# Optimization experiments

Measured on AMD Instinct MI355X. Metric: run time of the kernel, lower is better.

## Reference

```python
import jax, jax.numpy as jnp
import numpy as np

B, N, M, NF = 8, 512, 100, 42
DIMS = [NF, 256, 128, 64, 1]


def setup_inputs() -> dict:
    key = jax.random.key(0)
    ks = jax.random.split(key, 3 + len(DIMS) - 1)
    inp = {
        "image": jax.random.normal(ks[0], (B, N, NF), jnp.float32),
        "dfeat": jax.random.normal(ks[1], (B, N, M, NF, 3), jnp.float32) * 0.1,
        "neighbor": jax.random.randint(ks[2], (B, N, M), 0, N + 1),  # 0 = no neighbor, else 1-based atom idx
    }
    for l in range(len(DIMS) - 1):
        inp[f"W{l}"] = jax.random.normal(ks[3 + l], (DIMS[l], DIMS[l + 1]), jnp.float32) / np.sqrt(DIMS[l])
        inp[f"b{l}"] = jnp.zeros((DIMS[l + 1],), jnp.float32)
    return inp


def _atom_energy(x, Ws, bs):
    # per-atom MLP: sigmoid hidden layers, linear scalar output
    h = x
    for W, b in zip(Ws[:-1], bs[:-1]):
        h = jax.nn.sigmoid(h @ W + b)
    return (h @ Ws[-1] + bs[-1])[0]


def reference(image, dfeat, neighbor, W0, b0, W1, b1, W2, b2, W3, b3):
    Ws = (W0, W1, W2, W3)
    bs = (b0, b1, b2, b3)
    nb, na, nf = image.shape

    e_fn = lambda x: _atom_energy(x, Ws, bs)
    flat = image.reshape(-1, nf)
    Ei = jax.vmap(e_fn)(flat).reshape(nb, na)                      # [B, N]
    dE = jax.vmap(jax.grad(e_fn))(flat).reshape(nb, na, nf)        # dEi/dFeat, [B, N, F]
    Etot = jnp.sum(Ei, axis=1, keepdims=True)                      # [B, 1]

    # Force[b,i,:] = sum_m dE[b, neighbor[b,i,m]-1, :] @ dfeat[b,i,m,:,:], masking pad (0) entries
    mask = (neighbor > 0).astype(dE.dtype)                         # [B, N, M]
    idx = jnp.maximum(neighbor - 1, 0)                             # [B, N, M]
    dE_g = jax.vmap(lambda d, i: d[i])(dE, idx)                    # [B, N, M, F]
    Force = jnp.einsum('bnmf,bnmfd->bnd', dE_g * mask[..., None], dfeat)  # [B, N, 3]
    return Etot, Ei, Force
```

## Files before the change

### kernel.cpp

```cpp
#include <hip/hip_runtime.h>

#define NFEAT 42
#define H1 256
#define H2 128
#define H3 64
#define NB 8
#define NA 512
#define NM 100
#define TA 8

__device__ __forceinline__ float sigmoidf(float z) {
    return 1.0f / (1.0f + __expf(-z));
}

__global__ __launch_bounds__(256) void transpose_weights(
    const float* __restrict__ W0, const float* __restrict__ W1, const float* __restrict__ W2,
    float* __restrict__ W0T, float* __restrict__ W1T, float* __restrict__ W2T)
{
    int i = blockIdx.x * 256 + threadIdx.x;
    if (i < NFEAT * H1) {
        int f = i / H1, k = i - f * H1;
        W0T[k * NFEAT + f] = W0[i];
    }
    if (i < H1 * H2) {
        int k = i / H2, j = i - k * H2;
        W1T[j * H1 + k] = W1[i];
    }
    if (i < H2 * H3) {
        int j = i / H3, k = i - j * H3;
        W2T[k * H2 + j] = W2[i];
    }
}

__global__ __launch_bounds__(256) void mlp_fwd_bwd(
    const float* __restrict__ image,
    const float* __restrict__ W0, const float* __restrict__ b0,
    const float* __restrict__ W1, const float* __restrict__ b1,
    const float* __restrict__ W2, const float* __restrict__ b2,
    const float* __restrict__ W3, const float* __restrict__ b3,
    const float* __restrict__ W0T, const float* __restrict__ W1T, const float* __restrict__ W2T,
    float* __restrict__ Ei,
    float* __restrict__ dE)
{
    const int t = threadIdx.x;
    const int atom0 = blockIdx.x * TA;

    __shared__ float sx[TA][NFEAT];
    __shared__ __align__(16) float sh1[TA][H1];
    __shared__ __align__(16) float sh2[TA][H2];
    __shared__ __align__(16) float sh3[TA][H3];
    __shared__ __align__(16) float sd3[TA][H3];
    __shared__ __align__(16) float sd2[TA][H2];
    __shared__ __align__(16) float sd1[TA][H1];

    for (int i = t; i < TA * NFEAT; i += 256) {
        int a = i / NFEAT, f = i - a * NFEAT;
        sx[a][f] = image[(atom0 + a) * NFEAT + f];
    }
    __syncthreads();

    {
        float acc[TA];
        #pragma unroll
        for (int a = 0; a < TA; ++a) acc[a] = 0.f;
        for (int k = 0; k < NFEAT; ++k) {
            float w = W0[k * H1 + t];
            #pragma unroll
            for (int a = 0; a < TA; ++a) acc[a] += sx[a][k] * w;
        }
        float bb = b0[t];
        #pragma unroll
        for (int a = 0; a < TA; ++a) sh1[a][t] = sigmoidf(acc[a] + bb);
    }
    __syncthreads();

    {
        const int j = t & 127, g = t >> 7, a0 = g * 4;
        float acc[4] = {0.f, 0.f, 0.f, 0.f};
        for (int kk = 0; kk < H1 / 4; ++kk) {
            float w0_ = W1[(4 * kk + 0) * H2 + j];
            float w1_ = W1[(4 * kk + 1) * H2 + j];
            float w2_ = W1[(4 * kk + 2) * H2 + j];
            float w3_ = W1[(4 * kk + 3) * H2 + j];
            #pragma unroll
            for (int a = 0; a < 4; ++a) {
                float4 h = ((const float4*)sh1[a0 + a])[kk];
                acc[a] += h.x * w0_ + h.y * w1_ + h.z * w2_ + h.w * w3_;
            }
        }
        float bb = b1[j];
        #pragma unroll
        for (int a = 0; a < 4; ++a) sh2[a0 + a][j] = sigmoidf(acc[a] + bb);
    }
    __syncthreads();

    {
        const int j = t & 63, g = t >> 6, a0 = g * 2;
        float acc[2] = {0.f, 0.f};
        for (int kk = 0; kk < H2 / 4; ++kk) {
            float w0_ = W2[(4 * kk + 0) * H3 + j];
            float w1_ = W2[(4 * kk + 1) * H3 + j];
            float w2_ = W2[(4 * kk + 2) * H3 + j];
            float w3_ = W2[(4 * kk + 3) * H3 + j];
            #pragma unroll
            for (int a = 0; a < 2; ++a) {
                float4 h = ((const float4*)sh2[a0 + a])[kk];
                acc[a] += h.x * w0_ + h.y * w1_ + h.z * w2_ + h.w * w3_;
            }
        }
        float bb = b2[j];
        #pragma unroll
        for (int a = 0; a < 2; ++a) sh3[a0 + a][j] = sigmoidf(acc[a] + bb);
    }
    __syncthreads();

    {
        const int lane = t & 63, wv = t >> 6, a0 = wv * 2;
        float w = W3[lane];
        float bb = b3[0];
        #pragma unroll
        for (int a = a0; a < a0 + 2; ++a) {
            float h = sh3[a][lane];
            sd3[a][lane] = w * h * (1.f - h);
            float v = w * h;
            #pragma unroll
            for (int off = 32; off > 0; off >>= 1) v += __shfl_down(v, off, 64);
            if (lane == 0) Ei[atom0 + a] = v + bb;
        }
    }
    __syncthreads();

    {
        const int j = t & 127, g = t >> 7, a0 = g * 4;
        float acc[4] = {0.f, 0.f, 0.f, 0.f};
        for (int kk = 0; kk < H3 / 4; ++kk) {
            float w0_ = W2T[(4 * kk + 0) * H2 + j];
            float w1_ = W2T[(4 * kk + 1) * H2 + j];
            float w2_ = W2T[(4 * kk + 2) * H2 + j];
            float w3_ = W2T[(4 * kk + 3) * H2 + j];
            #pragma unroll
            for (int a = 0; a < 4; ++a) {
                float4 d = ((const float4*)sd3[a0 + a])[kk];
                acc[a] += d.x * w0_ + d.y * w1_ + d.z * w2_ + d.w * w3_;
            }
        }
        #pragma unroll
        for (int a = 0; a < 4; ++a) {
            float h = sh2[a0 + a][j];
            sd2[a0 + a][j] = acc[a] * h * (1.f - h);
        }
    }
    __syncthreads();

    {
        float acc[TA];
        #pragma unroll
        for (int a = 0; a < TA; ++a) acc[a] = 0.f;
        for (int jj = 0; jj < H2 / 4; ++jj) {
            float w0_ = W1T[(4 * jj + 0) * H1 + t];
            float w1_ = W1T[(4 * jj + 1) * H1 + t];
            float w2_ = W1T[(4 * jj + 2) * H1 + t];
            float w3_ = W1T[(4 * jj + 3) * H1 + t];
            #pragma unroll
            for (int a = 0; a < TA; ++a) {
                float4 d = ((const float4*)sd2[a])[jj];
                acc[a] += d.x * w0_ + d.y * w1_ + d.z * w2_ + d.w * w3_;
            }
        }
        #pragma unroll
        for (int a = 0; a < TA; ++a) {
            float h = sh1[a][t];
            sd1[a][t] = acc[a] * h * (1.f - h);
        }
    }
    __syncthreads();

    {
        const int f = t & 63, g = t >> 6, a0 = g * 2;
        if (f < NFEAT) {
            float acc[2] = {0.f, 0.f};
            for (int kk = 0; kk < H1 / 4; ++kk) {
                float w0_ = W0T[(4 * kk + 0) * NFEAT + f];
                float w1_ = W0T[(4 * kk + 1) * NFEAT + f];
                float w2_ = W0T[(4 * kk + 2) * NFEAT + f];
                float w3_ = W0T[(4 * kk + 3) * NFEAT + f];
                #pragma unroll
                for (int a = 0; a < 2; ++a) {
                    float4 d = ((const float4*)sd1[a0 + a])[kk];
                    acc[a] += d.x * w0_ + d.y * w1_ + d.z * w2_ + d.w * w3_;
                }
            }
            #pragma unroll
            for (int a = 0; a < 2; ++a)
                dE[(atom0 + a0 + a) * NFEAT + f] = acc[a];
        }
    }
}

__global__ __launch_bounds__(256) void etot_kernel(const float* __restrict__ Ei,
                                                   float* __restrict__ Etot)
{
    const int b = blockIdx.x;
    const int t = threadIdx.x;
    float v = Ei[b * NA + t] + Ei[b * NA + t + 256];
    __shared__ float red[4];
    #pragma unroll
    for (int off = 32; off > 0; off >>= 1) v += __shfl_down(v, off, 64);
    if ((t & 63) == 0) red[t >> 6] = v;
    __syncthreads();
    if (t == 0) Etot[b] = red[0] + red[1] + red[2] + red[3];
}

__global__ __launch_bounds__(256) void force_kernel(
    const float* __restrict__ dfeat,
    const int*   __restrict__ neighbor,
    const float* __restrict__ dE,
    float* __restrict__ Force)
{
    const int bi = blockIdx.x;
    const int b  = bi >> 9;
    const int t  = threadIdx.x;

    __shared__ int   s_nb[NM];
    __shared__ float s_dE[104 * NFEAT];
    __shared__ float s_part[1008];
    __shared__ float s_red[126];

    if (t < NM) s_nb[t] = neighbor[bi * NM + t];
    for (int i = t; i < 4 * NFEAT; i += 256) s_dE[NM * NFEAT + i] = 0.f;
    __syncthreads();

    for (int i = t; i < NM * NFEAT; i += 256) {
        int m = i / NFEAT, f = i - m * NFEAT;
        int n = s_nb[m];
        s_dE[i] = (n > 0) ? dE[((b << 9) + n - 1) * NFEAT + f] : 0.f;
    }
    __syncthreads();

    if (t < 252) {
        const int e4 = 4 * t;
        int off[4];
        #pragma unroll
        for (int c = 0; c < 4; ++c) {
            int ee = e4 + c;
            int r  = ee / 126;
            int e  = ee - r * 126;
            off[c] = r * NFEAT + e / 3;
        }
        const float* base = dfeat + (size_t)bi * (NM * NFEAT * 3);
        float acc[4] = {0.f, 0.f, 0.f, 0.f};

        for (int m0 = 0; m0 < 96; m0 += 8) {
            float4 v = *(const float4*)(base + m0 * 126 + e4);
            const float* sd = s_dE + m0 * NFEAT;
            acc[0] += v.x * sd[off[0]];
            acc[1] += v.y * sd[off[1]];
            acc[2] += v.z * sd[off[2]];
            acc[3] += v.w * sd[off[3]];
        }
        {
            const int m0 = 96;
            float vv[4];
            if (bi != NB * NA - 1) {
                float4 v = *(const float4*)(base + m0 * 126 + e4);
                vv[0] = v.x; vv[1] = v.y; vv[2] = v.z; vv[3] = v.w;
            } else {
                #pragma unroll
                for (int c = 0; c < 4; ++c) {
                    int r = (e4 + c) / 126;
                    vv[c] = (m0 + r < NM) ? base[m0 * 126 + e4 + c] : 0.f;
                }
            }
            const float* sd = s_dE + m0 * NFEAT;
            #pragma unroll
            for (int c = 0; c < 4; ++c) acc[c] += vv[c] * sd[off[c]];
        }
        #pragma unroll
        for (int c = 0; c < 4; ++c) s_part[e4 + c] = acc[c];
    }
    __syncthreads();

    if (t < 126) {
        float s = 0.f;
        #pragma unroll
        for (int r = 0; r < 8; ++r) s += s_part[r * 126 + t];
        s_red[t] = s;
    }
    __syncthreads();

    if (t < 3) {
        float s = 0.f;
        #pragma unroll
        for (int f = 0; f < NFEAT; ++f) s += s_red[f * 3 + t];
        Force[bi * 3 + t] = s;
    }
}

extern "C" void kernel_launch(void* const* d_in, const int* in_sizes, int n_in,
                              void* d_out, int out_size, void* d_ws, size_t ws_size,
                              hipStream_t stream) {
    const float* image    = (const float*)d_in[0];
    const float* dfeat    = (const float*)d_in[1];
    const int*   neighbor = (const int*)  d_in[2];
    const float* W0 = (const float*)d_in[3];
    const float* b0 = (const float*)d_in[4];
    const float* W1 = (const float*)d_in[5];
    const float* b1 = (const float*)d_in[6];
    const float* W2 = (const float*)d_in[7];
    const float* b2 = (const float*)d_in[8];
    const float* W3 = (const float*)d_in[9];
    const float* b3 = (const float*)d_in[10];

    float* out   = (float*)d_out;
    float* Etot  = out;
    float* Ei    = out + NB;
    float* Force = out + NB + NB * NA;

    float* dE  = (float*)d_ws;
    float* W0T = dE  + NB * NA * NFEAT;
    float* W1T = W0T + NFEAT * H1;
    float* W2T = W1T + H1 * H2;

    transpose_weights<<<(H1 * H2 + 255) / 256, 256, 0, stream>>>(W0, W1, W2, W0T, W1T, W2T);
    mlp_fwd_bwd<<<(NB * NA) / TA, 256, 0, stream>>>(image, W0, b0, W1, b1, W2, b2, W3, b3,
                                                    W0T, W1T, W2T, Ei, dE);
    etot_kernel<<<NB, 256, 0, stream>>>(Ei, Etot);
    force_kernel<<<NB * NA, 256, 0, stream>>>(dfeat, neighbor, dE, Force);
}
```

Before: 344.8 us.

## Halve atoms per MLP block, vectorize layer-0 loads, split force loop into two streams

Reduces atoms per block in the MLP forward/backward kernel from 8 to 4, doubling the grid and reassigning thread-to-atom mappings in each layer. The first layer now reads features as float4 from padded shared memory. The weight transpose kernel switches to coalesced writes with strided reads. The force kernel's main loop processes two independent m-halves per iteration to expose more memory-level parallelism. The cost is less weight reuse per block, so each weight load is amortized over fewer atoms.

```diff
diff --git a/kernel.cpp b/kernel.cpp
--- a/kernel.cpp
+++ b/kernel.cpp
@@ -7,7 +7,7 @@
 #define NB 8
 #define NA 512
 #define NM 100
-#define TA 8
+#define TA 4
 
 __device__ __forceinline__ float sigmoidf(float z) {
     return 1.0f / (1.0f + __expf(-z));
@@ -18,17 +18,17 @@
     float* __restrict__ W0T, float* __restrict__ W1T, float* __restrict__ W2T)
 {
     int i = blockIdx.x * 256 + threadIdx.x;
-    if (i < NFEAT * H1) {
-        int f = i / H1, k = i - f * H1;
-        W0T[k * NFEAT + f] = W0[i];
-    }
-    if (i < H1 * H2) {
-        int k = i / H2, j = i - k * H2;
-        W1T[j * H1 + k] = W1[i];
-    }
-    if (i < H2 * H3) {
-        int j = i / H3, k = i - j * H3;
-        W2T[k * H2 + j] = W2[i];
+    if (i < H1 * NFEAT) {
+        int k = i / NFEAT, f = i - k * NFEAT;
+        W0T[i] = W0[f * H1 + k];
+    }
+    if (i < H2 * H1) {
+        int j = i >> 8, k = i & 255;
+        W1T[i] = W1[k * H2 + j];
+    }
+    if (i < H3 * H2) {
+        int k = i >> 7, j = i & 127;
+        W2T[i] = W2[j * H3 + k];
     }
 }
 
@@ -45,7 +45,7 @@
     const int t = threadIdx.x;
     const int atom0 = blockIdx.x * TA;
 
-    __shared__ float sx[TA][NFEAT];
+    __shared__ __align__(16) float sx[TA][NFEAT + 2];
     __shared__ __align__(16) float sh1[TA][H1];
     __shared__ __align__(16) float sh2[TA][H2];
     __shared__ __align__(16) float sh3[TA][H3];
@@ -60,92 +60,91 @@
     __syncthreads();
 
     {
-        float acc[TA];
-        #pragma unroll
-        for (int a = 0; a < TA; ++a) acc[a] = 0.f;
-        for (int k = 0; k < NFEAT; ++k) {
-            float w = W0[k * H1 + t];
-            #pragma unroll
-            for (int a = 0; a < TA; ++a) acc[a] += sx[a][k] * w;
-        }
+        float acc[TA] = {0.f, 0.f, 0.f, 0.f};
+        for (int kk = 0; kk < 10; ++kk) {
+            float w0_ = W0[(4 * kk + 0) * H1 + t];
+            float w1_ = W0[(4 * kk + 1) * H1 + t];
+            float w2_ = W0[(4 * kk + 2) * H1 + t];
+            float w3_ = W0[(4 * kk + 3) * H1 + t];
+            #pragma unroll
+            for (int a = 0; a < TA; ++a) {
+                float4 h = ((const float4*)sx[a])[kk];
+                acc[a] += h.x * w0_ + h.y * w1_ + h.z * w2_ + h.w * w3_;
+            }
+        }
+        float wa = W0[40 * H1 + t], wb = W0[41 * H1 + t];
         float bb = b0[t];
         #pragma unroll
-        for (int a = 0; a < TA; ++a) sh1[a][t] = sigmoidf(acc[a] + bb);
-    }
-    __syncthreads();
-
-    {
-        const int j = t & 127, g = t >> 7, a0 = g * 4;
-        float acc[4] = {0.f, 0.f, 0.f, 0.f};
+        for (int a = 0; a < TA; ++a) {
+            acc[a] += sx[a][40] * wa + sx[a][41] * wb;
+            sh1[a][t] = sigmoidf(acc[a] + bb);
+        }
+    }
+    __syncthreads();
+
+    {
+        const int j = t & 127, a0 = (t >> 7) * 2;
+        float acc[2] = {0.f, 0.f};
         for (int kk = 0; kk < H1 / 4; ++kk) {
             float w0_ = W1[(4 * kk + 0) * H2 + j];
             float w1_ = W1[(4 * kk + 1) * H2 + j];
             float w2_ = W1[(4 * kk + 2) * H2 + j];
             float w3_ = W1[(4 * kk + 3) * H2 + j];
             #pragma unroll
-            for (int a = 0; a < 4; ++a) {
+            for (int a = 0; a < 2; ++a) {
                 float4 h = ((const float4*)sh1[a0 + a])[kk];
                 acc[a] += h.x * w0_ + h.y * w1_ + h.z * w2_ + h.w * w3_;
             }
         }
         float bb = b1[j];
         #pragma unroll
-        for (int a = 0; a < 4; ++a) sh2[a0 + a][j] = sigmoidf(acc[a] + bb);
-    }
-    __syncthreads();
-
-    {
-        const int j = t & 63, g = t >> 6, a0 = g * 2;
-        float acc[2] = {0.f, 0.f};
+        for (int a = 0; a < 2; ++a) sh2[a0 + a][j] = sigmoidf(acc[a] + bb);
+    }
+    __syncthreads();
+
+    {
+        const int j = t & 63, a = t >> 6;
+        float acc = 0.f;
         for (int kk = 0; kk < H2 / 4; ++kk) {
             float w0_ = W2[(4 * kk + 0) * H3 + j];
             float w1_ = W2[(4 * kk + 1) * H3 + j];
             float w2_ = W2[(4 * kk + 2) * H3 + j];
             float w3_ = W2[(4 * kk + 3) * H3 + j];
-            #pragma unroll
-            for (int a = 0; a < 2; ++a) {
-                float4 h = ((const float4*)sh2[a0 + a])[kk];
-                acc[a] += h.x * w0_ + h.y * w1_ + h.z * w2_ + h.w * w3_;
-            }
-        }
-        float bb = b2[j];
-        #pragma unroll
-        for (int a = 0; a < 2; ++a) sh3[a0 + a][j] = sigmoidf(acc[a] + bb);
-    }
-    __syncthreads();
-
-    {
-        const int lane = t & 63, wv = t >> 6, a0 = wv * 2;
+            float4 h = ((const float4*)sh2[a])[kk];
+            acc += h.x * w0_ + h.y * w1_ + h.z * w2_ + h.w * w3_;
+        }
+        sh3[a][j] = sigmoidf(acc + b2[j]);
+    }
+    __syncthreads();
+
+    {
+        const int lane = t & 63, a = t >> 6;
         float w = W3[lane];
-        float bb = b3[0];
-        #pragma unroll
-        for (int a = a0; a < a0 + 2; ++a) {
-            float h = sh3[a][lane];
-            sd3[a][lane] = w * h * (1.f - h);
-            float v = w * h;
-            #pragma unroll
-            for (int off = 32; off > 0; off >>= 1) v += __shfl_down(v, off, 64);
-            if (lane == 0) Ei[atom0 + a] = v + bb;
-        }
-    }
-    __syncthreads();
-
-    {
-        const int j = t & 127, g = t >> 7, a0 = g * 4;
-        float acc[4] = {0.f, 0.f, 0.f, 0.f};
+        float h = sh3[a][lane];
+        sd3[a][lane] = w * h * (1.f - h);
+        float v = w * h;
+        #pragma unroll
+        for (int off = 32; off > 0; off >>= 1) v += __shfl_down(v, off, 64);
+        if (lane == 0) Ei[atom0 + a] = v + b3[0];
+    }
+    __syncthreads();
+
+    {
+        const int j = t & 127, a0 = (t >> 7) * 2;
+        float acc[2] = {0.f, 0.f};
         for (int kk = 0; kk < H3 / 4; ++kk) {
             float w0_ = W2T[(4 * kk + 0) * H2 + j];
             float w1_ = W2T[(4 * kk + 1) * H2 + j];
             float w2_ = W2T[(4 * kk + 2) * H2 + j];
             float w3_ = W2T[(4 * kk + 3) * H2 + j];
             #pragma unroll
-            for (int a = 0; a < 4; ++a) {
+            for (int a = 0; a < 2; ++a) {
                 float4 d = ((const float4*)sd3[a0 + a])[kk];
                 acc[a] += d.x * w0_ + d.y * w1_ + d.z * w2_ + d.w * w3_;
             }
         }
         #pragma unroll
-        for (int a = 0; a < 4; ++a) {
+        for (int a = 0; a < 2; ++a) {
             float h = sh2[a0 + a][j];
             sd2[a0 + a][j] = acc[a] * h * (1.f - h);
         }
@@ -153,9 +152,7 @@
     __syncthreads();
 
     {
-        float acc[TA];
-        #pragma unroll
-        for (int a = 0; a < TA; ++a) acc[a] = 0.f;
+        float acc[TA] = {0.f, 0.f, 0.f, 0.f};
         for (int jj = 0; jj < H2 / 4; ++jj) {
             float w0_ = W1T[(4 * jj + 0) * H1 + t];
             float w1_ = W1T[(4 * jj + 1) * H1 + t];
@@ -176,23 +173,18 @@
     __syncthreads();
 
     {
-        const int f = t & 63, g = t >> 6, a0 = g * 2;
+        const int f = t & 63, a = t >> 6;
         if (f < NFEAT) {
-            float acc[2] = {0.f, 0.f};
+            float acc = 0.f;
             for (int kk = 0; kk < H1 / 4; ++kk) {
                 float w0_ = W0T[(4 * kk + 0) * NFEAT + f];
                 float w1_ = W0T[(4 * kk + 1) * NFEAT + f];
                 float w2_ = W0T[(4 * kk + 2) * NFEAT + f];
                 float w3_ = W0T[(4 * kk + 3) * NFEAT + f];
-                #pragma unroll
-                for (int a = 0; a < 2; ++a) {
-                    float4 d = ((const float4*)sd1[a0 + a])[kk];
-                    acc[a] += d.x * w0_ + d.y * w1_ + d.z * w2_ + d.w * w3_;
-                }
-            }
-            #pragma unroll
-            for (int a = 0; a < 2; ++a)
-                dE[(atom0 + a0 + a) * NFEAT + f] = acc[a];
+                float4 d = ((const float4*)sd1[a])[kk];
+                acc += d.x * w0_ + d.y * w1_ + d.z * w2_ + d.w * w3_;
+            }
+            dE[(atom0 + a) * NFEAT + f] = acc;
         }
     }
 }
@@ -250,13 +242,15 @@
         const float* base = dfeat + (size_t)bi * (NM * NFEAT * 3);
         float acc[4] = {0.f, 0.f, 0.f, 0.f};
 
-        for (int m0 = 0; m0 < 96; m0 += 8) {
-            float4 v = *(const float4*)(base + m0 * 126 + e4);
-            const float* sd = s_dE + m0 * NFEAT;
-            acc[0] += v.x * sd[off[0]];
-            acc[1] += v.y * sd[off[1]];
-            acc[2] += v.z * sd[off[2]];
-            acc[3] += v.w * sd[off[3]];
+        for (int m0 = 0; m0 < 48; m0 += 8) {
+            float4 vA = *(const float4*)(base + m0 * 126 + e4);
+            float4 vB = *(const float4*)(base + (m0 + 48) * 126 + e4);
+            const float* sdA = s_dE + m0 * NFEAT;
+            const float* sdB = s_dE + (m0 + 48) * NFEAT;
+            acc[0] += vA.x * sdA[off[0]] + vB.x * sdB[off[0]];
+            acc[1] += vA.y * sdA[off[1]] + vB.y * sdB[off[1]];
+            acc[2] += vA.z * sdA[off[2]] + vB.z * sdB[off[2]];
+            acc[3] += vA.w * sdA[off[3]] + vB.w * sdB[off[3]];
         }
         {
             const int m0 = 96;
@@ -318,8 +312,8 @@
 
     float* dE  = (float*)d_ws;
     float* W0T = dE  + NB * NA * NFEAT;
-    float* W1T = W0T + NFEAT * H1;
-    float* W2T = W1T + H1 * H2;
+    float* W1T = W0T + H1 * NFEAT;
+    float* W2T = W1T + H2 * H1;
 
     transpose_weights<<<(H1 * H2 + 255) / 256, 256, 0, stream>>>(W0, W1, W2, W0T, W1T, W2T);
     mlp_fwd_bwd<<<(NB * NA) / TA, 256, 0, stream>>>(image, W0, b0, W1, b1, W2, b2, W3, b3,
```

Result: no change. 346.6 us (+0.5%).
